# Kernel tuning notes

Measured on AMD Instinct MI355X. Metric: run time of the kernel, lower is better.

Reference implementation:

```python
import jax, jax.numpy as jnp
import numpy as np

N_NODES = 64000
N_GRAPHS = 128


def _sage_conv(x, edge_index, Wl, Wr, b):
    # PyG SAGEConv (mean aggregator): out = lin_l(mean_{j in N(i)} x_j) + lin_r(x_i)
    src, dst = edge_index[0], edge_index[1]
    msg = x[src]                                   # [E, d] gather
    s = jax.ops.segment_sum(msg, dst, num_segments=N_NODES)          # [N, d]
    cnt = jax.ops.segment_sum(jnp.ones(src.shape, x.dtype), dst,
                              num_segments=N_NODES)[:, None]          # [N, 1]
    aggr = jnp.where(cnt > 0, s / jnp.maximum(cnt, 1.0), jnp.zeros((), x.dtype))
    return aggr @ Wl.T + x @ Wr.T + b


def setup_inputs() -> dict:
    key = jax.random.key(0)
    ks = jax.random.split(key, 9)
    E = 1024000
    x = jax.random.normal(ks[0], (N_NODES, 64), dtype=jnp.float32)
    edge_index = jax.random.randint(ks[1], (2, E), 0, N_NODES, dtype=jnp.int64)
    batch = jnp.sort(jax.random.randint(ks[2], (N_NODES,), 0, N_GRAPHS, dtype=jnp.int64))
    sc = 1.0 / np.sqrt(64.0)
    Wl = jax.random.normal(ks[3], (3, 64, 64), dtype=jnp.float32) * sc
    Wr = jax.random.normal(ks[4], (3, 64, 64), dtype=jnp.float32) * sc
    b = jax.random.normal(ks[5], (3, 64), dtype=jnp.float32) * sc
    Wl_out = jax.random.normal(ks[6], (2, 64), dtype=jnp.float32) * sc
    Wr_out = jax.random.normal(ks[7], (2, 64), dtype=jnp.float32) * sc
    b_out = jax.random.normal(ks[8], (2,), dtype=jnp.float32) * sc
    return {"x": x, "edge_index": edge_index, "batch": batch,
            "Wl": Wl, "Wr": Wr, "b": b,
            "Wl_out": Wl_out, "Wr_out": Wr_out, "b_out": b_out}


def reference(x, edge_index, batch, Wl, Wr, b, Wl_out, Wr_out, b_out):
    h = x
    for i in range(Wl.shape[0]):  # fixed n_layers=3 hidden SAGEConv layers
        h = _sage_conv(h, edge_index, Wl[i], Wr[i], b[i])
        # dropout is identity at inference
        h = jax.nn.relu(h)
    h = _sage_conv(h, edge_index, Wl_out, Wr_out, b_out)  # [N, n_classes]
    # global mean pool over graphs in the batch
    s = jax.ops.segment_sum(h, batch, num_segments=N_GRAPHS)
    cnt = jax.ops.segment_sum(jnp.ones((N_NODES,), h.dtype), batch,
                              num_segments=N_GRAPHS)[:, None]
    return s / jnp.maximum(cnt, 1.0)
```

## Files before the change

### kernel.cpp

```cpp
#include <hip/hip_runtime.h>

#define NNODES 64000
#define NGRAPHS 128
#define D 64
#define TP 72
#define NT 250
#define ESEG 5120
#define ZG 1024
#define NPOOL 8
#define CGRID 2000

typedef _Float16 half8 __attribute__((ext_vector_type(8)));
typedef float f32x4 __attribute__((ext_vector_type(4)));

__device__ __forceinline__ int lower_bound(const int* __restrict__ a, int n, int key) {
    int lo = 0, hi = n;
    while (lo < hi) {
        int mid = (lo + hi) >> 1;
        if (a[mid] < key) lo = mid + 1; else hi = mid;
    }
    return lo;
}

__global__ __launch_bounds__(256) void convert_partition(
        const float4* __restrict__ x, half8* __restrict__ xh, int n8,
        const float* __restrict__ Wl, const float* __restrict__ Wr,
        _Float16* __restrict__ Wlh, _Float16* __restrict__ Wrh,
        const int* __restrict__ src, const int* __restrict__ dst, int E,
        int* __restrict__ ecur, int2* __restrict__ elist,
        float* __restrict__ pool, int PB) {
    __shared__ int bcnt[256], bbase[256];
    int tid = threadIdx.x;
    if ((int)blockIdx.x < PB) {
        const int U = 16;
        int base = blockIdx.x * 256 * U;
        bcnt[tid] = 0;
        __syncthreads();
        int2 ed[U]; int team[U], slot[U];
#pragma unroll
        for (int u = 0; u < U; ++u) {
            int e = base + tid + u * 256;
            team[u] = -1;
            if (e < E) {
                int s = __builtin_nontemporal_load(src + e);
                int d = __builtin_nontemporal_load(dst + e);
                ed[u] = make_int2(s, d);
                team[u] = d >> 8;
                slot[u] = atomicAdd(&bcnt[team[u]], 1);
            }
        }
        __syncthreads();
        if (bcnt[tid] > 0) bbase[tid] = atomicAdd(&ecur[tid], bcnt[tid]);
        __syncthreads();
#pragma unroll
        for (int u = 0; u < U; ++u)
            if (team[u] >= 0)
                elist[(size_t)team[u] * ESEG + bbase[team[u]] + slot[u]] = ed[u];
    } else {
        int bid = blockIdx.x - PB;
        int i = bid * 256 + tid;
        int st = CGRID * 256;
        for (; i < n8; i += st) {
            float4 a = x[2 * i], b = x[2 * i + 1];
            half8 o;
            o[0] = (_Float16)a.x; o[1] = (_Float16)a.y; o[2] = (_Float16)a.z; o[3] = (_Float16)a.w;
            o[4] = (_Float16)b.x; o[5] = (_Float16)b.y; o[6] = (_Float16)b.z; o[7] = (_Float16)b.w;
            xh[i] = o;
        }
        int j = bid * 256 + tid;
        if (j < 3 * D * D) {
            Wlh[j] = (_Float16)Wl[j];
            Wrh[j] = (_Float16)Wr[j];
        }
        if (bid == 0) {
#pragma unroll
            for (int k = 0; k < NPOOL; ++k) pool[k * 256 + tid] = 0.f;
        }
    }
}

__global__ __launch_bounds__(1024) void fill_block(
        const int2* __restrict__ elist, const int* __restrict__ ecur,
        const int* __restrict__ batch,
        int* __restrict__ offs, int2* __restrict__ info, int* __restrict__ col) {
    __shared__ int2 els[ESEG];
    __shared__ int lhist[256], lofs[256];
    int team = blockIdx.x;
    int t = threadIdx.x;
    int n = ecur[team];
    const int2* el = elist + (size_t)team * ESEG;

    if (t < 256) lofs[t] = (t < NT) ? ecur[t] : 0;
    __syncthreads();
    for (int off = 1; off < 256; off <<= 1) {
        int x = 0;
        if (t < 256 && t >= off) x = lofs[t - off];
        __syncthreads();
        if (t < 256) lofs[t] += x;
        __syncthreads();
    }
    int tb = (team > 0) ? lofs[team - 1] : 0;
    if (team == NT - 1 && t == 0) offs[NNODES] = lofs[NT - 1];
    __syncthreads();

    if (t < 256) lhist[t] = 0;
    __syncthreads();
    for (int e = t; e < n; e += 1024) {
        int2 ed = el[e];
        els[e] = ed;
        atomicAdd(&lhist[ed.y & 255], 1);
    }
    __syncthreads();
    if (t < 256) lofs[t] = lhist[t];
    __syncthreads();
    for (int off = 1; off < 256; off <<= 1) {
        int x = 0;
        if (t < 256 && t >= off) x = lofs[t - off];
        __syncthreads();
        if (t < 256) lofs[t] += x;
        __syncthreads();
    }
    if (t < 256) {
        int v = lhist[t];
        int ex = lofs[t] - v;
        int gi = team * 256 + t;
        offs[gi] = tb + ex;
        float inv = (v > 0) ? 1.f / (float)v : 0.f;
        info[gi] = make_int2(batch[gi], __float_as_int(inv));
        lofs[t] = ex;
    }
    __syncthreads();
    for (int e = t; e < n; e += 1024) {
        int2 ed = els[e];
        int p = tb + atomicAdd(&lofs[ed.y & 255], 1);
        col[p] = ed.x;
    }
}

template <int PRJ>
__global__ __launch_bounds__(256) void layer_fused(
        const _Float16* __restrict__ h, _Float16* __restrict__ out,
        const int* __restrict__ offs, const int* __restrict__ col,
        const _Float16* __restrict__ Wlh, const _Float16* __restrict__ Wrh,
        const float* __restrict__ b,
        const float* __restrict__ Wlo, const float* __restrict__ Wro,
        float* __restrict__ z12, float* __restrict__ z34) {
    __shared__ _Float16 tile[4][16][TP];
    int lane = threadIdx.x & 63;
    int w    = threadIdx.x >> 6;
    int row0 = (blockIdx.x * 4 + w) * 16;

    {
        int ns  = lane >> 2;
        int ch2 = lane & 3;
        int i = row0 + ns;
        int beg = offs[i], end = offs[i + 1];
        half8 s0 = {0, 0, 0, 0, 0, 0, 0, 0};
        half8 s1 = {0, 0, 0, 0, 0, 0, 0, 0};
        int e = beg;
        for (; e + 8 <= end; e += 8) {
            int c0 = col[e],     c1 = col[e + 1], c2 = col[e + 2], c3 = col[e + 3];
            int c4 = col[e + 4], c5 = col[e + 5], c6 = col[e + 6], c7 = col[e + 7];
            const _Float16* r0 = h + (size_t)c0 * D + ch2 * 16;
            const _Float16* r1 = h + (size_t)c1 * D + ch2 * 16;
            const _Float16* r2 = h + (size_t)c2 * D + ch2 * 16;
            const _Float16* r3 = h + (size_t)c3 * D + ch2 * 16;
            const _Float16* r4 = h + (size_t)c4 * D + ch2 * 16;
            const _Float16* r5 = h + (size_t)c5 * D + ch2 * 16;
            const _Float16* r6 = h + (size_t)c6 * D + ch2 * 16;
            const _Float16* r7 = h + (size_t)c7 * D + ch2 * 16;
            half8 a0 = *(const half8*)r0,       a1 = *(const half8*)r1;
            half8 a2 = *(const half8*)r2,       a3 = *(const half8*)r3;
            half8 a4 = *(const half8*)r4,       a5 = *(const half8*)r5;
            half8 a6 = *(const half8*)r6,       a7 = *(const half8*)r7;
            half8 b0 = *(const half8*)(r0 + 8), b1 = *(const half8*)(r1 + 8);
            half8 b2 = *(const half8*)(r2 + 8), b3 = *(const half8*)(r3 + 8);
            half8 b4 = *(const half8*)(r4 + 8), b5 = *(const half8*)(r5 + 8);
            half8 b6 = *(const half8*)(r6 + 8), b7 = *(const half8*)(r7 + 8);
            s0 += ((a0 + a1) + (a2 + a3)) + ((a4 + a5) + (a6 + a7));
            s1 += ((b0 + b1) + (b2 + b3)) + ((b4 + b5) + (b6 + b7));
        }
        for (; e + 4 <= end; e += 4) {
            int c0 = col[e], c1 = col[e + 1], c2 = col[e + 2], c3 = col[e + 3];
            const _Float16* r0 = h + (size_t)c0 * D + ch2 * 16;
            const _Float16* r1 = h + (size_t)c1 * D + ch2 * 16;
            const _Float16* r2 = h + (size_t)c2 * D + ch2 * 16;
            const _Float16* r3 = h + (size_t)c3 * D + ch2 * 16;
            half8 a0 = *(const half8*)r0,       a1 = *(const half8*)r1;
            half8 a2 = *(const half8*)r2,       a3 = *(const half8*)r3;
            half8 b0 = *(const half8*)(r0 + 8), b1 = *(const half8*)(r1 + 8);
            half8 b2 = *(const half8*)(r2 + 8), b3 = *(const half8*)(r3 + 8);
            s0 += (a0 + a1) + (a2 + a3);
            s1 += (b0 + b1) + (b2 + b3);
        }
        for (; e < end; ++e) {
            const _Float16* rp = h + (size_t)col[e] * D + ch2 * 16;
            s0 += *(const half8*)rp;
            s1 += *(const half8*)(rp + 8);
        }
        float inv = (end > beg) ? 1.f / (float)(end - beg) : 0.f;
        half8 o0, o1;
#pragma unroll
        for (int j = 0; j < 8; ++j) {
            o0[j] = (_Float16)((float)s0[j] * inv);
            o1[j] = (_Float16)((float)s1[j] * inv);
        }
        *(half8*)(&tile[w][ns][ch2 * 16])     = o0;
        *(half8*)(&tile[w][ns][ch2 * 16 + 8]) = o1;
    }

    int r = lane & 15;
    int g = lane >> 4;

    half8 bf[4][4];
#pragma unroll
    for (int kt = 0; kt < 4; ++kt) {
        const _Float16* Wm = (kt < 2) ? Wlh : Wrh;
        int kk = (kt & 1) * 32 + g * 8;
#pragma unroll
        for (int nt = 0; nt < 4; ++nt)
            bf[kt][nt] = *(const half8*)(Wm + (size_t)(nt * 16 + r) * D + kk);
    }

    f32x4 acc[4];
#pragma unroll
    for (int nt = 0; nt < 4; ++nt) {
        float bv = b[nt * 16 + r];
        acc[nt] = (f32x4){bv, bv, bv, bv};
    }

#pragma unroll
    for (int kt = 0; kt < 4; ++kt) {
        int kk = (kt & 1) * 32 + g * 8;
        half8 af;
        if (kt < 2) af = *(const half8*)(&tile[w][r][kk]);
        else        af = *(const half8*)(h + (size_t)(row0 + r) * D + kk);
#pragma unroll
        for (int nt = 0; nt < 4; ++nt)
            acc[nt] = __builtin_amdgcn_mfma_f32_16x16x32_f16(af, bf[kt][nt], acc[nt], 0, 0, 0);
    }

    if (!PRJ) {
#pragma unroll
        for (int nt = 0; nt < 4; ++nt)
#pragma unroll
            for (int q = 0; q < 4; ++q) {
                int row = row0 + g * 4 + q;
                out[(size_t)row * D + nt * 16 + r] = (_Float16)fmaxf(acc[nt][q], 0.f);
            }
    } else {
#pragma unroll
        for (int nt = 0; nt < 4; ++nt)
#pragma unroll
            for (int q = 0; q < 4; ++q)
                tile[w][g * 4 + q][nt * 16 + r] = (_Float16)fmaxf(acc[nt][q], 0.f);

        half8 pf[2];
#pragma unroll
        for (int kt = 0; kt < 2; ++kt) {
            half8 t = {0, 0, 0, 0, 0, 0, 0, 0};
            if (r < 4) {
                const float* Pr = (r < 2) ? (Wlo + r * D) : (Wro + (r - 2) * D);
                int kk = kt * 32 + g * 8;
#pragma unroll
                for (int j = 0; j < 8; ++j) t[j] = (_Float16)Pr[kk + j];
            }
            pf[kt] = t;
        }
        f32x4 az = (f32x4){0.f, 0.f, 0.f, 0.f};
#pragma unroll
        for (int kt = 0; kt < 2; ++kt) {
            half8 af = *(const half8*)(&tile[w][r][kt * 32 + g * 8]);
            az = __builtin_amdgcn_mfma_f32_16x16x32_f16(af, pf[kt], az, 0, 0, 0);
        }
#pragma unroll
        for (int q = 0; q < 4; ++q) {
            int row = row0 + g * 4 + q;
            if (r < 2)      z12[row * 2 + r]       = az[q];
            else if (r < 4) z34[row * 2 + (r - 2)] = az[q];
        }
    }
}

__global__ __launch_bounds__(256) void zpool_edge(
        const float2* __restrict__ z12, const float2* __restrict__ z34,
        const int* __restrict__ src, const int* __restrict__ dst,
        const int2* __restrict__ info, int E, float* __restrict__ pool) {
    __shared__ float lp[NGRAPHS * 2];
    int t = threadIdx.x;
    lp[t] = 0.f;
    __syncthreads();
    int tid = blockIdx.x * blockDim.x + t;
    int stride = gridDim.x * blockDim.x;
    for (int e = tid; e < E; e += stride) {
        int s = __builtin_nontemporal_load(src + e);
        int d = __builtin_nontemporal_load(dst + e);
        float2 z = z12[s];
        int2 nf = info[d];
        float w = __int_as_float(nf.y);
        atomicAdd(&lp[0 * NGRAPHS + nf.x], z.x * w);
        atomicAdd(&lp[1 * NGRAPHS + nf.x], z.y * w);
    }
    for (int i = tid; i < NNODES; i += stride) {
        float2 zi = z34[i];
        int g = info[i].x;
        atomicAdd(&lp[0 * NGRAPHS + g], zi.x);
        atomicAdd(&lp[1 * NGRAPHS + g], zi.y);
    }
    __syncthreads();
    float v = lp[t];
    if (v != 0.f) atomicAdd(&pool[(blockIdx.x & (NPOOL - 1)) * 256 + t], v);
}

__global__ void out_kernel(const float* __restrict__ pool, const int* __restrict__ batch,
                           const float* __restrict__ bo, float* __restrict__ out) {
    int t = threadIdx.x;
    float v = 0.f;
#pragma unroll
    for (int k = 0; k < NPOOL; ++k) v += pool[k * 256 + t];
    int j = t >> 7, g = t & 127;
    int c = lower_bound(batch, NNODES, g + 1) - lower_bound(batch, NNODES, g);
    out[g * 2 + j] = (c > 0) ? v / (float)c + bo[j] : 0.f;
}


extern "C" void kernel_launch(void* const* d_in, const int* in_sizes, int n_in,
                              void* d_out, int out_size, void* d_ws, size_t ws_size,
                              hipStream_t stream) {
    const float* x    = (const float*)d_in[0];
    const int*   eidx = (const int*)d_in[1];
    const int*   batch= (const int*)d_in[2];
    const float* Wl   = (const float*)d_in[3];
    const float* Wr   = (const float*)d_in[4];
    const float* b    = (const float*)d_in[5];
    const float* Wlo  = (const float*)d_in[6];
    const float* Wro  = (const float*)d_in[7];
    const float* bo   = (const float*)d_in[8];

    int E = in_sizes[1] / 2;
    const int* src = eidx;
    const int* dst = eidx + E;

    char* ws = (char*)d_ws;
    size_t hb = (size_t)NNODES * D * 2;
    _Float16* xh   = (_Float16*)ws;
    _Float16* bufA = (_Float16*)(ws + hb);
    char* p = ws + 2 * hb;
    _Float16* Wlh  = (_Float16*)p;  p += 3 * D * D * 2;
    _Float16* Wrh  = (_Float16*)p;  p += 3 * D * D * 2;
    int*    col  = (int*)p;     p += (size_t)E * 4;
    int*    offs = (int*)p;     p += ((size_t)(NNODES + 1) * 4 + 127) / 128 * 128;
    int2*   info = (int2*)p;    p += (size_t)NNODES * 8;
    float*  z12  = (float*)p;   p += (size_t)NNODES * 8;
    float*  z34  = (float*)p;   p += (size_t)NNODES * 8;
    int*    ecur = (int*)p;     p += 1024;
    float*  pool = (float*)p;   p += NPOOL * 256 * 4;
    int2*   elist= (int2*)p;

    hipMemsetAsync(ecur, 0, 1024, stream);

    int PB = (E + 4095) / 4096;
    convert_partition<<<PB + CGRID, 256, 0, stream>>>(
        (const float4*)x, (half8*)xh, NNODES * D / 8,
        Wl, Wr, Wlh, Wrh, src, dst, E, ecur, elist, pool, PB);

    fill_block<<<NT, 1024, 0, stream>>>(elist, ecur, batch, offs, info, col);

    layer_fused<0><<<1000, 256, 0, stream>>>(xh,   bufA, offs, col,
                                             Wlh,             Wrh,             b,
                                             nullptr, nullptr, nullptr, nullptr);
    layer_fused<0><<<1000, 256, 0, stream>>>(bufA, xh,   offs, col,
                                             Wlh + D * D,     Wrh + D * D,     b + D,
                                             nullptr, nullptr, nullptr, nullptr);
    layer_fused<1><<<1000, 256, 0, stream>>>(xh,   bufA, offs, col,
                                             Wlh + 2 * D * D, Wrh + 2 * D * D, b + 2 * D,
                                             Wlo, Wro, z12, z34);

    zpool_edge<<<ZG, 256, 0, stream>>>((const float2*)z12, (const float2*)z34,
                                       src, dst, info, E, pool);
    out_kernel<<<1, 256, 0, stream>>>(pool, batch, bo, (float*)d_out);
}
```

Baseline: 136.6 us.

## Pool root-term in last layer and read partitioned edge list for edge pooling

The per-node root projection (z34) is no longer written to global memory. It is accumulated into per-graph shared-memory bins inside the final layer kernel and flushed to the pool buffer there. The edge-pooling kernel now reads the pre-partitioned int2 edge list (elist/ecur) instead of the raw src/dst arrays, so each edge costs one 8-byte load instead of two separate index loads. This drops the z34 round trip and the node loop from the pooling kernel. In exchange the last layer gains extra syncthreads and shared atomics, and the edge kernel depends on the elist layout built during partitioning.

```diff
diff --git a/kernel.cpp b/kernel.cpp
--- a/kernel.cpp
+++ b/kernel.cpp
@@ -6,7 +6,6 @@
 #define TP 72
 #define NT 250
 #define ESEG 5120
-#define ZG 1024
 #define NPOOL 8
 #define CGRID 2000
 
@@ -144,11 +143,14 @@
         const _Float16* __restrict__ Wlh, const _Float16* __restrict__ Wrh,
         const float* __restrict__ b,
         const float* __restrict__ Wlo, const float* __restrict__ Wro,
-        float* __restrict__ z12, float* __restrict__ z34) {
+        float* __restrict__ z12, const int2* __restrict__ info,
+        float* __restrict__ pool) {
     __shared__ _Float16 tile[4][16][TP];
+    __shared__ float bins[256];
     int lane = threadIdx.x & 63;
     int w    = threadIdx.x >> 6;
     int row0 = (blockIdx.x * 4 + w) * 16;
+    if (PRJ) bins[threadIdx.x] = 0.f;
 
     {
         int ns  = lane >> 2;
@@ -276,36 +278,43 @@
 #pragma unroll
         for (int q = 0; q < 4; ++q) {
             int row = row0 + g * 4 + q;
-            if (r < 2)      z12[row * 2 + r]       = az[q];
-            else if (r < 4) z34[row * 2 + (r - 2)] = az[q];
-        }
-    }
-}
-
-__global__ __launch_bounds__(256) void zpool_edge(
-        const float2* __restrict__ z12, const float2* __restrict__ z34,
-        const int* __restrict__ src, const int* __restrict__ dst,
-        const int2* __restrict__ info, int E, float* __restrict__ pool) {
+            if (r < 2) z12[row * 2 + r] = az[q];
+        }
+        __syncthreads();
+        if (r >= 2 && r < 4) {
+            int j = r - 2;
+#pragma unroll
+            for (int q = 0; q < 4; ++q) {
+                int row = row0 + g * 4 + q;
+                atomicAdd(&bins[j * NGRAPHS + info[row].x], az[q]);
+            }
+        }
+        __syncthreads();
+        float v = bins[threadIdx.x];
+        if (v != 0.f)
+            atomicAdd(&pool[(blockIdx.x & (NPOOL - 1)) * 256 + threadIdx.x], v);
+    }
+}
+
+__global__ __launch_bounds__(256) void zpool_team(
+        const float2* __restrict__ z12, const int2* __restrict__ elist,
+        const int* __restrict__ ecur, const int2* __restrict__ info,
+        float* __restrict__ pool) {
     __shared__ float lp[NGRAPHS * 2];
     int t = threadIdx.x;
     lp[t] = 0.f;
     __syncthreads();
-    int tid = blockIdx.x * blockDim.x + t;
-    int stride = gridDim.x * blockDim.x;
-    for (int e = tid; e < E; e += stride) {
-        int s = __builtin_nontemporal_load(src + e);
-        int d = __builtin_nontemporal_load(dst + e);
-        float2 z = z12[s];
-        int2 nf = info[d];
+    int team = blockIdx.x >> 2;
+    int part = blockIdx.x & 3;
+    int n = ecur[team];
+    const int2* el = elist + (size_t)team * ESEG;
+    for (int e = part * 256 + t; e < n; e += 1024) {
+        int2 ed = el[e];
+        float2 z = z12[ed.x];
+        int2 nf = info[ed.y];
         float w = __int_as_float(nf.y);
         atomicAdd(&lp[0 * NGRAPHS + nf.x], z.x * w);
         atomicAdd(&lp[1 * NGRAPHS + nf.x], z.y * w);
-    }
-    for (int i = tid; i < NNODES; i += stride) {
-        float2 zi = z34[i];
-        int g = info[i].x;
-        atomicAdd(&lp[0 * NGRAPHS + g], zi.x);
-        atomicAdd(&lp[1 * NGRAPHS + g], zi.y);
     }
     __syncthreads();
     float v = lp[t];
@@ -352,7 +361,6 @@
     int*    offs = (int*)p;     p += ((size_t)(NNODES + 1) * 4 + 127) / 128 * 128;
     int2*   info = (int2*)p;    p += (size_t)NNODES * 8;
     float*  z12  = (float*)p;   p += (size_t)NNODES * 8;
-    float*  z34  = (float*)p;   p += (size_t)NNODES * 8;
     int*    ecur = (int*)p;     p += 1024;
     float*  pool = (float*)p;   p += NPOOL * 256 * 4;
     int2*   elist= (int2*)p;
@@ -368,15 +376,14 @@
 
     layer_fused<0><<<1000, 256, 0, stream>>>(xh,   bufA, offs, col,
                                              Wlh,             Wrh,             b,
-                                             nullptr, nullptr, nullptr, nullptr);
+                                             nullptr, nullptr, nullptr, nullptr, nullptr);
     layer_fused<0><<<1000, 256, 0, stream>>>(bufA, xh,   offs, col,
                                              Wlh + D * D,     Wrh + D * D,     b + D,
-                                             nullptr, nullptr, nullptr, nullptr);
+                                             nullptr, nullptr, nullptr, nullptr, nullptr);
     layer_fused<1><<<1000, 256, 0, stream>>>(xh,   bufA, offs, col,
                                              Wlh + 2 * D * D, Wrh + 2 * D * D, b + 2 * D,
-                                             Wlo, Wro, z12, z34);
-
-    zpool_edge<<<ZG, 256, 0, stream>>>((const float2*)z12, (const float2*)z34,
-                                       src, dst, info, E, pool);
+                                             Wlo, Wro, z12, info, pool);
+
+    zpool_team<<<NT * 4, 256, 0, stream>>>((const float2*)z12, elist, ecur, info, pool);
     out_kernel<<<1, 256, 0, stream>>>(pool, batch, bo, (float*)d_out);
 }
```

After: 137.6 us. Within noise of the previous version (+0.7%).
